# Optimization experiments

Hardware: AMD Instinct MI355X
Metric: run time of the kernel (lower is better)

## Reference

```python
import jax, jax.numpy as jnp
import numpy as np

C_IN = 256
C_RED = max(4, C_IN // 4)  # 64


def setup_inputs() -> dict:
    key = jax.random.key(0)
    k1, k2, k3, k4, k5 = jax.random.split(key, 5)
    B, C, H, W = 4, C_IN, 64, 64
    x = jax.random.normal(k1, (B, C, H, W), dtype=jnp.float32)
    # 1x1 convs (no bias) are just channel matmuls: weight shape (out_ch, in_ch)
    s_in = 1.0 / np.sqrt(C)
    s_red = 1.0 / np.sqrt(C_RED)
    Wq = jax.random.normal(k2, (C_RED, C), dtype=jnp.float32) * s_in
    Wk = jax.random.normal(k3, (C_RED, C), dtype=jnp.float32) * s_in
    Wv = jax.random.normal(k4, (C_RED, C), dtype=jnp.float32) * s_in
    Wp = jax.random.normal(k5, (C, C_RED), dtype=jnp.float32) * s_red
    return {"x": x, "Wq": Wq, "Wk": Wk, "Wv": Wv, "Wp": Wp}


def reference(x, Wq, Wk, Wv, Wp):
    B, C, H, W = x.shape
    N = H * W
    xf = x.reshape(B, C, N)                       # (B, C, N)
    q = jnp.einsum('rc,bcn->bnr', Wq, xf)         # (B, N, c_red)
    k = jnp.einsum('rc,bcn->brn', Wk, xf)         # (B, c_red, N)
    v = jnp.einsum('rc,bcn->bnr', Wv, xf)         # (B, N, c_red)
    scale = 1.0 / jnp.sqrt(jnp.float32(k.shape[1]))
    attn = jnp.einsum('bnr,brm->bnm', q, k) * scale   # (B, N, N)
    attn = jax.nn.softmax(attn, axis=-1)
    out = jnp.einsum('bnm,bmr->brn', attn, v)     # (B, c_red, N)
    out = jnp.einsum('cr,brn->bcn', Wp, out)      # (B, C, N)
    return out.reshape(B, C, H, W) + x
```

## Files before the change

kernel.cpp:

```cpp
#include <hip/hip_runtime.h>
#include <hip/hip_bf16.h>

#define CIN 256
#define CRED 64
#define NB 4
#define NN 4096

typedef float v4f __attribute__((ext_vector_type(4)));
typedef short v8s __attribute__((ext_vector_type(8)));
typedef unsigned short u16;
typedef u16 u16x4 __attribute__((ext_vector_type(4)));
typedef u16 u16x8 __attribute__((ext_vector_type(8)));
typedef unsigned int u32;

#define LOG2E 1.4426950408889634f

__device__ __forceinline__ u16 f2bf(float f) {
    union { float f; u32 u; } v; v.f = f;
    u32 r = (v.u + 0x7FFFu + ((v.u >> 16) & 1u)) >> 16;
    return (u16)r;
}
__device__ __forceinline__ float bf2f(u16 s) {
    union { u32 u; float f; } v; v.u = ((u32)s) << 16;
    return v.f;
}
__device__ __forceinline__ u32 pkbf(float a, float b) {
    float2 f; f.x = a; f.y = b;
    __hip_bfloat162 h = __float22bfloat162_rn(f);
    union { __hip_bfloat162 h; u32 u; } c; c.h = h;
    return c.u;
}
__device__ __forceinline__ v4f mfma16(v8s a, v8s b, v4f c) {
    return __builtin_amdgcn_mfma_f32_16x16x32_bf16(a, b, c, 0, 0, 0);
}
__device__ __forceinline__ float fexp2(float x) {
#if __has_builtin(__builtin_amdgcn_exp2f)
    return __builtin_amdgcn_exp2f(x);
#else
    return exp2f(x);
#endif
}

__global__ __launch_bounds__(256) void k_wconv(const float* __restrict__ Wq,
                                               const float* __restrict__ Wk,
                                               const float* __restrict__ Wv,
                                               const float* __restrict__ Wp,
                                               u16* __restrict__ Wb,
                                               u16* __restrict__ WpB) {
    int t = threadIdx.x;
    if (blockIdx.x < 48) {
        int idx = (blockIdx.x * 256 + t) * 4;
        int row = idx >> 8;
        int mat = row >> 6, r = row & 63, col = idx & 255;
        const float* src = (mat == 0) ? Wq : (mat == 1) ? Wk : Wv;
        float4 v = *(const float4*)&src[r * 256 + col];
        float s = (mat == 0) ? (0.125f * LOG2E) : 1.0f;
        u16x4 o;
        o[0] = f2bf(v.x * s); o[1] = f2bf(v.y * s);
        o[2] = f2bf(v.z * s); o[3] = f2bf(v.w * s);
        *(u16x4*)&Wb[idx] = o;
    } else {
        int idx = ((blockIdx.x - 48) * 256 + t) * 4;
        float4 v = *(const float4*)&Wp[idx];
        u16x4 o;
        o[0] = f2bf(v.x); o[1] = f2bf(v.y);
        o[2] = f2bf(v.z); o[3] = f2bf(v.w);
        *(u16x4*)&WpB[idx] = o;
    }
}

__global__ __launch_bounds__(256) void k_qkvm(const float* __restrict__ x,
                                              const u16* __restrict__ Wb,
                                              u16* __restrict__ Q, u16* __restrict__ K,
                                              u16* __restrict__ V) {
    int t = threadIdx.x;
    int wv = t >> 6, lane = t & 63, c15 = lane & 15, quad = lane >> 4;
    int n0g = blockIdx.x * 32;
    int b = n0g >> 12, nb = n0g & 4095;
    const float* xb = x + ((size_t)b << 20);

    v8s Af[2][8];
#pragma unroll
    for (int nt = 0; nt < 2; ++nt) {
        const float* px = xb + nb + nt * 16 + c15 + (size_t)quad * 8 * 4096;
#pragma unroll
        for (int kc = 0; kc < 8; ++kc) {
            float f[8];
#pragma unroll
            for (int j = 0; j < 8; ++j)
                f[j] = px[((size_t)kc * 32 + j) * 4096];
            union { v8s s; u32 w[4]; } pk;
            pk.w[0] = pkbf(f[0], f[1]); pk.w[1] = pkbf(f[2], f[3]);
            pk.w[2] = pkbf(f[4], f[5]); pk.w[3] = pkbf(f[6], f[7]);
            Af[nt][kc] = pk.s;
        }
    }

#pragma unroll
    for (int rti = 0; rti < 3; ++rti) {
        int rt = wv * 3 + rti;
        const u16* wrow = Wb + (size_t)(rt * 16 + c15) * 256 + quad * 8;
        v8s Bf[8];
#pragma unroll
        for (int kc = 0; kc < 8; ++kc) Bf[kc] = *(const v8s*)&wrow[kc * 32];
#pragma unroll
        for (int nt = 0; nt < 2; ++nt) {
            v4f acc = {0.f, 0.f, 0.f, 0.f};
#pragma unroll
            for (int kc = 0; kc < 8; ++kc)
                acc = mfma16(Af[nt][kc], Bf[kc], acc);
            if (rt < 8) {
                u16* base = (rt < 4) ? Q : K;
                u16* dst = base + ((size_t)b << 18)
                         + (size_t)(nb + nt * 16 + quad * 4) * 64
                         + (rt & 3) * 16 + c15;
#pragma unroll
                for (int g = 0; g < 4; ++g) dst[g * 64] = f2bf(acc[g]);
            } else {
                int hi2 = ((nb + nt * 16) >> 4) & 3;
                size_t base = ((size_t)b * 64 + (rt - 8) * 16 + c15) * 4096
                            + (size_t)((nb + nt * 16) & ~63) + hi2;
#pragma unroll
                for (int g = 0; g < 4; ++g)
                    V[base + (quad * 4 + g) * 4] = f2bf(acc[g]);
            }
        }
    }
}

__global__ __launch_bounds__(256, 4) void k_flash(const u16* __restrict__ Q,
                                                  const u16* __restrict__ K,
                                                  const u16* __restrict__ V,
                                                  u16* __restrict__ OP,
                                                  float* __restrict__ Lb,
                                                  int sh) {
    __shared__ u16 Kl[64][72];
    __shared__ u16 Vl[64][72];
    __shared__ u16 Pl[4][32][72];
    int t = threadIdx.x;
    int p = blockIdx.x & ((1u << sh) - 1);
    int tile = blockIdx.x >> sh;
    int b = tile >> 5;
    int n0 = (tile & 31) * 128;
    int wv = t >> 6;
    int lane = t & 63;
    int c15 = lane & 15;
    int quad = lane >> 4;
    int nw = n0 + wv * 32;
    const u16* Qb = Q + (size_t)b * NN * 64;
    const u16* Kb = K + (size_t)b * NN * 64;
    const u16* Vb = V + (size_t)b * 64 * NN;

    v8s Qa[2][2];
#pragma unroll
    for (int rg = 0; rg < 2; ++rg)
#pragma unroll
        for (int c2 = 0; c2 < 2; ++c2)
            Qa[rg][c2] = *(const v8s*)&Qb[(size_t)(nw + rg * 16 + c15) * 64 + c2 * 32 + quad * 8];

    v4f O[2][4];
    float ls[2][4];
#pragma unroll
    for (int rg = 0; rg < 2; ++rg)
#pragma unroll
        for (int g = 0; g < 4; ++g) {
            ls[rg][g] = 0.f;
#pragma unroll
            for (int cg = 0; cg < 4; ++cg) O[rg][cg][g] = 0.f;
        }

    int mlen = NN >> sh;
    int m0 = p * mlen;
    int iters = mlen >> 6;
    int srow = t >> 3, scol = (t & 7) * 8;

    v8s kpre[2], vpre[2];
#pragma unroll
    for (int pass = 0; pass < 2; ++pass) {
        int rr = srow + pass * 32;
        kpre[pass] = *(const v8s*)&Kb[(size_t)(m0 + rr) * 64 + scol];
        vpre[pass] = *(const v8s*)&Vb[(size_t)rr * NN + m0 + scol];
    }

    for (int it = 0; it < iters; ++it) {
#pragma unroll
        for (int pass = 0; pass < 2; ++pass) {
            int rr = srow + pass * 32;
            *(v8s*)&Kl[rr][scol] = kpre[pass];
            *(v8s*)&Vl[rr][scol] = vpre[pass];
        }
        __syncthreads();

        if (it + 1 < iters) {
            int mt = m0 + (it + 1) * 64;
#pragma unroll
            for (int pass = 0; pass < 2; ++pass) {
                int rr = srow + pass * 32;
                kpre[pass] = *(const v8s*)&Kb[(size_t)(mt + rr) * 64 + scol];
                vpre[pass] = *(const v8s*)&Vb[(size_t)rr * NN + mt + scol];
            }
        }

        v4f S[2][4];
#pragma unroll
        for (int rg = 0; rg < 2; ++rg)
#pragma unroll
            for (int s = 0; s < 4; ++s)
#pragma unroll
                for (int g = 0; g < 4; ++g) S[rg][s][g] = 0.f;
#pragma unroll
        for (int s = 0; s < 4; ++s)
#pragma unroll
            for (int c2 = 0; c2 < 2; ++c2) {
                v8s kb = *(const v8s*)&Kl[s * 16 + c15][c2 * 32 + quad * 8];
                S[0][s] = mfma16(Qa[0][c2], kb, S[0][s]);
                S[1][s] = mfma16(Qa[1][c2], kb, S[1][s]);
            }

#pragma unroll
        for (int rg = 0; rg < 2; ++rg) {
            float E[4][4];
#pragma unroll
            for (int s = 0; s < 4; ++s)
#pragma unroll
                for (int g = 0; g < 4; ++g) {
                    float e = fexp2(S[rg][s][g]);
                    E[s][g] = e;
                    ls[rg][g] += e;
                }
#pragma unroll
            for (int g = 0; g < 4; ++g) {
                union { u16x4 v; u32 w[2]; } p2;
                p2.w[0] = pkbf(E[0][g], E[1][g]);
                p2.w[1] = pkbf(E[2][g], E[3][g]);
                *(u16x4*)&Pl[wv][rg * 16 + quad * 4 + g][c15 * 4] = p2.v;
            }
        }

        v8s Pa[2][2];
#pragma unroll
        for (int rg = 0; rg < 2; ++rg)
#pragma unroll
            for (int c2 = 0; c2 < 2; ++c2)
                Pa[rg][c2] = *(const v8s*)&Pl[wv][rg * 16 + c15][c2 * 32 + quad * 8];
#pragma unroll
        for (int cg = 0; cg < 4; ++cg)
#pragma unroll
            for (int c2 = 0; c2 < 2; ++c2) {
                v8s vb = *(const v8s*)&Vl[cg * 16 + c15][c2 * 32 + quad * 8];
                O[0][cg] = mfma16(Pa[0][c2], vb, O[0][cg]);
                O[1][cg] = mfma16(Pa[1][c2], vb, O[1][cg]);
            }
        __syncthreads();
    }

    u16* OPp = OP + (size_t)p * (NB * NN * 64) + (size_t)b * NN * 64;
#pragma unroll
    for (int rg = 0; rg < 2; ++rg)
#pragma unroll
        for (int cg = 0; cg < 4; ++cg)
#pragma unroll
            for (int g = 0; g < 4; ++g) {
                int n = nw + rg * 16 + quad * 4 + g;
                OPp[(size_t)n * 64 + cg * 16 + c15] = f2bf(O[rg][cg][g]);
            }
#pragma unroll
    for (int rg = 0; rg < 2; ++rg)
#pragma unroll
        for (int g = 0; g < 4; ++g) {
            float v = ls[rg][g];
#pragma unroll
            for (int off = 1; off <= 8; off <<= 1) v += __shfl_xor(v, off);
            ls[rg][g] = v;
        }
    if (c15 == 0) {
        float* Lp = Lb + (size_t)p * (NB * NN) + (size_t)b * NN;
#pragma unroll
        for (int rg = 0; rg < 2; ++rg)
#pragma unroll
            for (int g = 0; g < 4; ++g) {
                int n = nw + rg * 16 + quad * 4 + g;
                Lp[n] = ls[rg][g];
            }
    }
}

#define OMP 72
__global__ __launch_bounds__(256) void k_proj(const u16* __restrict__ OP,
                                              const float* __restrict__ Lb,
                                              const u16* __restrict__ WpB,
                                              const float* __restrict__ x,
                                              float* __restrict__ out,
                                              int nsp) {
    __shared__ u16 Om[16 * OMP];
    int t = threadIdx.x;
    int b = blockIdx.x >> 8;
    int n0 = (blockIdx.x & 255) * 16;

    {
        int n_l = t >> 4, r0 = (t & 15) * 4;
        size_t nidx = (size_t)b * NN + n0 + n_l;
        float o[4] = {0.f, 0.f, 0.f, 0.f};
        float l = 0.f;
        for (int p = 0; p < nsp; ++p) {
            u16x4 u = *(const u16x4*)&OP[((size_t)p * (NB * NN) + nidx) * 64 + r0];
#pragma unroll
            for (int j = 0; j < 4; ++j) o[j] += bf2f(u[j]);
            l += Lb[(size_t)p * (NB * NN) + nidx];
        }
        float inv = 1.0f / l;
        union { u16x4 v; u32 w[2]; } p2;
        p2.w[0] = pkbf(o[0] * inv, o[1] * inv);
        p2.w[1] = pkbf(o[2] * inv, o[3] * inv);
        *(u16x4*)&Om[n_l * OMP + r0] = p2.v;
    }
    __syncthreads();

    int lane = t & 63, wvv = t >> 6, c15 = lane & 15, quad = lane >> 4;
    v8s B0 = *(const v8s*)&Om[c15 * OMP + quad * 8];
    v8s B1 = *(const v8s*)&Om[c15 * OMP + 32 + quad * 8];
#pragma unroll
    for (int ct0 = 0; ct0 < 4; ++ct0) {
        int ct = wvv * 4 + ct0;
        const u16* wrow = WpB + (size_t)(ct * 16 + c15) * 64 + quad * 8;
        v8s A0 = *(const v8s*)&wrow[0];
        v8s A1 = *(const v8s*)&wrow[32];
        v4f acc = {0.f, 0.f, 0.f, 0.f};
        acc = mfma16(A0, B0, acc);
        acc = mfma16(A1, B1, acc);
        size_t base = ((size_t)(b * 256 + ct * 16 + quad * 4)) * 4096 + n0 + c15;
#pragma unroll
        for (int g = 0; g < 4; ++g)
            out[base + (size_t)g * 4096] = acc[g] + x[base + (size_t)g * 4096];
    }
}

extern "C" void kernel_launch(void* const* d_in, const int* in_sizes, int n_in,
                              void* d_out, int out_size, void* d_ws, size_t ws_size,
                              hipStream_t stream) {
    const float* x  = (const float*)d_in[0];
    const float* Wq = (const float*)d_in[1];
    const float* Wk = (const float*)d_in[2];
    const float* Wv = (const float*)d_in[3];
    const float* Wp = (const float*)d_in[4];
    float* out = (float*)d_out;
    char* ws = (char*)d_ws;

    int nsp = (ws_size >= (size_t)24 * 1024 * 1024) ? 8 : 4;
    int sh = (nsp == 8) ? 3 : 2;

    u16* Wb  = (u16*)(ws);
    u16* WpB = (u16*)(ws + 131072);
    u16* Q   = (u16*)(ws + 262144);
    u16* K   = (u16*)(ws + 262144 + 2097152);
    u16* V   = (u16*)(ws + 262144 + 2 * 2097152);
    u16* OP  = (u16*)(ws + 262144 + 3 * 2097152);
    float* Lbuf = (float*)(ws + 262144 + (size_t)(3 + nsp) * 2097152);

    k_wconv<<<64, 256, 0, stream>>>(Wq, Wk, Wv, Wp, Wb, WpB);
    k_qkvm<<<512, 256, 0, stream>>>(x, Wb, Q, K, V);
    k_flash<<<NB * 32 * nsp, 256, 0, stream>>>(Q, K, V, OP, Lbuf, sh);
    k_proj<<<NB * 256, 256, 0, stream>>>(OP, Lbuf, WpB, x, out, nsp);
}
```

Baseline: 126.1 us.

## Fuse four attention kernels into one cooperative kernel with grid syncs

Replaces the four separate launches (weight conversion, QKV projection, flash attention, output projection) with one cooperative kernel of 1024 blocks that uses grid.sync between phases. This is meant to remove the launch gaps and tail idle time between kernels. It requires all 1024 blocks to be co-resident (launch_bounds 256,4), and it falls back to the old path if the cooperative launch fails. Grid-wide barriers add their own cost, and idle blocks wait during the smaller phases.

```diff
diff --git a/kernel.cpp b/kernel.cpp
--- a/kernel.cpp
+++ b/kernel.cpp
@@ -1,5 +1,8 @@
 #include <hip/hip_runtime.h>
 #include <hip/hip_bf16.h>
+#include <hip/hip_cooperative_groups.h>
+
+namespace cg = cooperative_groups;
 
 #define CIN 256
 #define CRED 64
@@ -39,6 +42,293 @@
 #else
     return exp2f(x);
 #endif
+}
+
+__global__ __launch_bounds__(256, 4) void k_fused(
+    const float* __restrict__ x, const float* __restrict__ Wq,
+    const float* __restrict__ Wk, const float* __restrict__ Wv,
+    const float* __restrict__ Wp, u16* __restrict__ Wb, u16* __restrict__ WpB,
+    u16* __restrict__ Q, u16* __restrict__ K, u16* __restrict__ V,
+    u16* __restrict__ OP, float* __restrict__ Lb, float* __restrict__ out) {
+    __shared__ u16 Kl[64][72];
+    __shared__ u16 Vl[64][72];
+    __shared__ u16 Pl[4][32][72];
+    cg::grid_group grid = cg::this_grid();
+    const int t = threadIdx.x;
+    const int bid = blockIdx.x;
+    const int sh = 3;
+
+    if (bid < 64) {
+        if (bid < 48) {
+            int idx = (bid * 256 + t) * 4;
+            int row = idx >> 8;
+            int mat = row >> 6, r = row & 63, col = idx & 255;
+            const float* src = (mat == 0) ? Wq : (mat == 1) ? Wk : Wv;
+            float4 v = *(const float4*)&src[r * 256 + col];
+            float s = (mat == 0) ? (0.125f * LOG2E) : 1.0f;
+            u16x4 o;
+            o[0] = f2bf(v.x * s); o[1] = f2bf(v.y * s);
+            o[2] = f2bf(v.z * s); o[3] = f2bf(v.w * s);
+            *(u16x4*)&Wb[idx] = o;
+        } else {
+            int idx = ((bid - 48) * 256 + t) * 4;
+            float4 v = *(const float4*)&Wp[idx];
+            u16x4 o;
+            o[0] = f2bf(v.x); o[1] = f2bf(v.y);
+            o[2] = f2bf(v.z); o[3] = f2bf(v.w);
+            *(u16x4*)&WpB[idx] = o;
+        }
+    }
+    grid.sync();
+
+    if (bid < 512) {
+        int wv = t >> 6, lane = t & 63, c15 = lane & 15, quad = lane >> 4;
+        int n0g = bid * 32;
+        int b = n0g >> 12, nb = n0g & 4095;
+        const float* xb = x + ((size_t)b << 20);
+
+        v8s Af[2][8];
+#pragma unroll
+        for (int nt = 0; nt < 2; ++nt) {
+            const float* px = xb + nb + nt * 16 + c15 + (size_t)quad * 8 * 4096;
+#pragma unroll
+            for (int kc = 0; kc < 8; ++kc) {
+                float f[8];
+#pragma unroll
+                for (int j = 0; j < 8; ++j)
+                    f[j] = px[((size_t)kc * 32 + j) * 4096];
+                union { v8s s; u32 w[4]; } pk;
+                pk.w[0] = pkbf(f[0], f[1]); pk.w[1] = pkbf(f[2], f[3]);
+                pk.w[2] = pkbf(f[4], f[5]); pk.w[3] = pkbf(f[6], f[7]);
+                Af[nt][kc] = pk.s;
+            }
+        }
+#pragma unroll
+        for (int rti = 0; rti < 3; ++rti) {
+            int rt = wv * 3 + rti;
+            const u16* wrow = Wb + (size_t)(rt * 16 + c15) * 256 + quad * 8;
+            v8s Bf[8];
+#pragma unroll
+            for (int kc = 0; kc < 8; ++kc) Bf[kc] = *(const v8s*)&wrow[kc * 32];
+#pragma unroll
+            for (int nt = 0; nt < 2; ++nt) {
+                v4f acc = {0.f, 0.f, 0.f, 0.f};
+#pragma unroll
+                for (int kc = 0; kc < 8; ++kc)
+                    acc = mfma16(Af[nt][kc], Bf[kc], acc);
+                if (rt < 8) {
+                    u16* base = (rt < 4) ? Q : K;
+                    u16* dst = base + ((size_t)b << 18)
+                             + (size_t)(nb + nt * 16 + quad * 4) * 64
+                             + (rt & 3) * 16 + c15;
+#pragma unroll
+                    for (int g = 0; g < 4; ++g) dst[g * 64] = f2bf(acc[g]);
+                } else {
+                    int hi2 = ((nb + nt * 16) >> 4) & 3;
+                    size_t base = ((size_t)b * 64 + (rt - 8) * 16 + c15) * 4096
+                                + (size_t)((nb + nt * 16) & ~63) + hi2;
+#pragma unroll
+                    for (int g = 0; g < 4; ++g)
+                        V[base + (quad * 4 + g) * 4] = f2bf(acc[g]);
+                }
+            }
+        }
+    }
+    grid.sync();
+
+    {
+        int p = bid & ((1u << sh) - 1);
+        int tile = bid >> sh;
+        int b = tile >> 5;
+        int n0 = (tile & 31) * 128;
+        int wv = t >> 6;
+        int lane = t & 63;
+        int c15 = lane & 15;
+        int quad = lane >> 4;
+        int nw = n0 + wv * 32;
+        const u16* Qb = Q + (size_t)b * NN * 64;
+        const u16* Kb = K + (size_t)b * NN * 64;
+        const u16* Vb = V + (size_t)b * 64 * NN;
+
+        v8s Qa[2][2];
+#pragma unroll
+        for (int rg = 0; rg < 2; ++rg)
+#pragma unroll
+            for (int c2 = 0; c2 < 2; ++c2)
+                Qa[rg][c2] = *(const v8s*)&Qb[(size_t)(nw + rg * 16 + c15) * 64 + c2 * 32 + quad * 8];
+
+        v4f O[2][4];
+        float ls[2][4];
+#pragma unroll
+        for (int rg = 0; rg < 2; ++rg)
+#pragma unroll
+            for (int g = 0; g < 4; ++g) {
+                ls[rg][g] = 0.f;
+#pragma unroll
+                for (int cg2 = 0; cg2 < 4; ++cg2) O[rg][cg2][g] = 0.f;
+            }
+
+        int mlen = NN >> sh;
+        int m0 = p * mlen;
+        int iters = mlen >> 6;
+        int srow = t >> 3, scol = (t & 7) * 8;
+
+        v8s kpre[2], vpre[2];
+#pragma unroll
+        for (int pass = 0; pass < 2; ++pass) {
+            int rr = srow + pass * 32;
+            kpre[pass] = *(const v8s*)&Kb[(size_t)(m0 + rr) * 64 + scol];
+            vpre[pass] = *(const v8s*)&Vb[(size_t)rr * NN + m0 + scol];
+        }
+
+        for (int it = 0; it < iters; ++it) {
+#pragma unroll
+            for (int pass = 0; pass < 2; ++pass) {
+                int rr = srow + pass * 32;
+                *(v8s*)&Kl[rr][scol] = kpre[pass];
+                *(v8s*)&Vl[rr][scol] = vpre[pass];
+            }
+            __syncthreads();
+
+            if (it + 1 < iters) {
+                int mt = m0 + (it + 1) * 64;
+#pragma unroll
+                for (int pass = 0; pass < 2; ++pass) {
+                    int rr = srow + pass * 32;
+                    kpre[pass] = *(const v8s*)&Kb[(size_t)(mt + rr) * 64 + scol];
+                    vpre[pass] = *(const v8s*)&Vb[(size_t)rr * NN + mt + scol];
+                }
+            }
+
+            v4f S[2][4];
+#pragma unroll
+            for (int rg = 0; rg < 2; ++rg)
+#pragma unroll
+                for (int s = 0; s < 4; ++s)
+#pragma unroll
+                    for (int g = 0; g < 4; ++g) S[rg][s][g] = 0.f;
+#pragma unroll
+            for (int s = 0; s < 4; ++s)
+#pragma unroll
+                for (int c2 = 0; c2 < 2; ++c2) {
+                    v8s kb = *(const v8s*)&Kl[s * 16 + c15][c2 * 32 + quad * 8];
+                    S[0][s] = mfma16(Qa[0][c2], kb, S[0][s]);
+                    S[1][s] = mfma16(Qa[1][c2], kb, S[1][s]);
+                }
+
+#pragma unroll
+            for (int rg = 0; rg < 2; ++rg) {
+                float E[4][4];
+#pragma unroll
+                for (int s = 0; s < 4; ++s)
+#pragma unroll
+                    for (int g = 0; g < 4; ++g) {
+                        float e = fexp2(S[rg][s][g]);
+                        E[s][g] = e;
+                        ls[rg][g] += e;
+                    }
+#pragma unroll
+                for (int g = 0; g < 4; ++g) {
+                    union { u16x4 v; u32 w[2]; } p2;
+                    p2.w[0] = pkbf(E[0][g], E[1][g]);
+                    p2.w[1] = pkbf(E[2][g], E[3][g]);
+                    *(u16x4*)&Pl[wv][rg * 16 + quad * 4 + g][c15 * 4] = p2.v;
+                }
+            }
+
+            v8s Pa[2][2];
+#pragma unroll
+            for (int rg = 0; rg < 2; ++rg)
+#pragma unroll
+                for (int c2 = 0; c2 < 2; ++c2)
+                    Pa[rg][c2] = *(const v8s*)&Pl[wv][rg * 16 + c15][c2 * 32 + quad * 8];
+#pragma unroll
+            for (int cg2 = 0; cg2 < 4; ++cg2)
+#pragma unroll
+                for (int c2 = 0; c2 < 2; ++c2) {
+                    v8s vb = *(const v8s*)&Vl[cg2 * 16 + c15][c2 * 32 + quad * 8];
+                    O[0][cg2] = mfma16(Pa[0][c2], vb, O[0][cg2]);
+                    O[1][cg2] = mfma16(Pa[1][c2], vb, O[1][cg2]);
+                }
+            __syncthreads();
+        }
+
+        u16* OPp = OP + (size_t)p * (NB * NN * 64) + (size_t)b * NN * 64;
+#pragma unroll
+        for (int rg = 0; rg < 2; ++rg)
+#pragma unroll
+            for (int cg2 = 0; cg2 < 4; ++cg2)
+#pragma unroll
+                for (int g = 0; g < 4; ++g) {
+                    int n = nw + rg * 16 + quad * 4 + g;
+                    OPp[(size_t)n * 64 + cg2 * 16 + c15] = f2bf(O[rg][cg2][g]);
+                }
+#pragma unroll
+        for (int rg = 0; rg < 2; ++rg)
+#pragma unroll
+            for (int g = 0; g < 4; ++g) {
+                float v = ls[rg][g];
+#pragma unroll
+                for (int off = 1; off <= 8; off <<= 1) v += __shfl_xor(v, off);
+                ls[rg][g] = v;
+            }
+        if (c15 == 0) {
+            float* Lp = Lb + (size_t)p * (NB * NN) + (size_t)b * NN;
+#pragma unroll
+            for (int rg = 0; rg < 2; ++rg)
+#pragma unroll
+                for (int g = 0; g < 4; ++g) {
+                    int n = nw + rg * 16 + quad * 4 + g;
+                    Lp[n] = ls[rg][g];
+                }
+        }
+    }
+    grid.sync();
+
+    {
+        const int OMP = 72;
+        u16* Om = &Pl[0][0][0];
+        int nsp = 1 << sh;
+        int b = bid >> 8;
+        int n0 = (bid & 255) * 16;
+
+        {
+            int n_l = t >> 4, r0 = (t & 15) * 4;
+            size_t nidx = (size_t)b * NN + n0 + n_l;
+            float o[4] = {0.f, 0.f, 0.f, 0.f};
+            float l = 0.f;
+            for (int p = 0; p < nsp; ++p) {
+                u16x4 u = *(const u16x4*)&OP[((size_t)p * (NB * NN) + nidx) * 64 + r0];
+#pragma unroll
+                for (int j = 0; j < 4; ++j) o[j] += bf2f(u[j]);
+                l += Lb[(size_t)p * (NB * NN) + nidx];
+            }
+            float inv = 1.0f / l;
+            union { u16x4 v; u32 w[2]; } p2;
+            p2.w[0] = pkbf(o[0] * inv, o[1] * inv);
+            p2.w[1] = pkbf(o[2] * inv, o[3] * inv);
+            *(u16x4*)&Om[n_l * OMP + r0] = p2.v;
+        }
+        __syncthreads();
+
+        int lane = t & 63, wvv = t >> 6, c15 = lane & 15, quad = lane >> 4;
+        v8s B0 = *(const v8s*)&Om[c15 * OMP + quad * 8];
+        v8s B1 = *(const v8s*)&Om[c15 * OMP + 32 + quad * 8];
+#pragma unroll
+        for (int ct0 = 0; ct0 < 4; ++ct0) {
+            int ct = wvv * 4 + ct0;
+            const u16* wrow = WpB + (size_t)(ct * 16 + c15) * 64 + quad * 8;
+            v8s A0 = *(const v8s*)&wrow[0];
+            v8s A1 = *(const v8s*)&wrow[32];
+            v4f acc = {0.f, 0.f, 0.f, 0.f};
+            acc = mfma16(A0, B0, acc);
+            acc = mfma16(A1, B1, acc);
+            size_t base = ((size_t)(b * 256 + ct * 16 + quad * 4)) * 4096 + n0 + c15;
+#pragma unroll
+            for (int g = 0; g < 4; ++g)
+                out[base + (size_t)g * 4096] = acc[g] + x[base + (size_t)g * 4096];
+        }
+    }
 }
 
 __global__ __launch_bounds__(256) void k_wconv(const float* __restrict__ Wq,
@@ -95,7 +385,6 @@
             Af[nt][kc] = pk.s;
         }
     }
-
 #pragma unroll
     for (int rti = 0; rti < 3; ++rti) {
         int rt = wv * 3 + rti;
@@ -357,8 +646,20 @@
     u16* OP  = (u16*)(ws + 262144 + 3 * 2097152);
     float* Lbuf = (float*)(ws + 262144 + (size_t)(3 + nsp) * 2097152);
 
-    k_wconv<<<64, 256, 0, stream>>>(Wq, Wk, Wv, Wp, Wb, WpB);
-    k_qkvm<<<512, 256, 0, stream>>>(x, Wb, Q, K, V);
-    k_flash<<<NB * 32 * nsp, 256, 0, stream>>>(Q, K, V, OP, Lbuf, sh);
-    k_proj<<<NB * 256, 256, 0, stream>>>(OP, Lbuf, WpB, x, out, nsp);
-}
+    bool done = false;
+    if (nsp == 8) {
+        void* args[] = {(void*)&x, (void*)&Wq, (void*)&Wk, (void*)&Wv, (void*)&Wp,
+                        (void*)&Wb, (void*)&WpB, (void*)&Q, (void*)&K, (void*)&V,
+                        (void*)&OP, (void*)&Lbuf, (void*)&out};
+        hipError_t e = hipLaunchCooperativeKernel((const void*)k_fused,
+                                                  dim3(1024), dim3(256),
+                                                  args, 0, stream);
+        done = (e == hipSuccess);
+    }
+    if (!done) {
+        k_wconv<<<64, 256, 0, stream>>>(Wq, Wk, Wv, Wp, Wb, WpB);
+        k_qkvm<<<512, 256, 0, stream>>>(x, Wb, Q, K, V);
+        k_flash<<<NB * 32 * nsp, 256, 0, stream>>>(Q, K, V, OP, Lbuf, sh);
+        k_proj<<<NB * 256, 256, 0, stream>>>(OP, Lbuf, WpB, x, out, nsp);
+    }
+}
```

New measurement: 441.0 us. +249.8%, slower.
